# Performance work log

Measured on AMD Instinct MI355X. Metric: run time of the kernel, lower is better.

Reference implementation:

```python
import jax, jax.numpy as jnp
import numpy as np

B, S, D = 8, 1024, 768
H, DK, DV = 12, 64, 64
NEG = -1e12


def setup_inputs() -> dict:
    key = jax.random.key(0)
    ks = jax.random.split(key, 8)
    s = 0.02
    return {
        "x": jax.random.normal(ks[0], (B, S, D), jnp.float32),
        "Wq": jax.random.normal(ks[1], (D, H * DK), jnp.float32) * s,
        "bq": jnp.zeros((H * DK,), jnp.float32),
        "Wk": jax.random.normal(ks[2], (D, H * DK), jnp.float32) * s,
        "bk": jnp.zeros((H * DK,), jnp.float32),
        "Wv": jax.random.normal(ks[3], (D, H * DV), jnp.float32) * s,
        "bv": jnp.zeros((H * DV,), jnp.float32),
        "Wo": jax.random.normal(ks[4], (H * DV, D), jnp.float32) * s,
        "bo": jnp.zeros((D,), jnp.float32),
        "position_bias": jax.random.normal(ks[5], (S, S, DK), jnp.float32) * s,
        "q_mask": jnp.ones((B, S), jnp.float32),
        "v_mask": jnp.ones((B, S), jnp.float32),
    }


def reference(x, Wq, bq, Wk, bk, Wv, bv, Wo, bo, position_bias, q_mask, v_mask):
    b, s, _ = x.shape
    qw = (x @ Wq + bq).reshape(b, s, H, DK)  # [b,s,h,dk]
    kw = (x @ Wk + bk).reshape(b, s, H, DK)
    vw = (x @ Wv + bv).reshape(b, s, H, DV)
    # scores with fused typical_relative position bias
    a = jnp.einsum("bjhd,bkhd->bhjk", qw, kw)
    a = a + jnp.einsum("bjhd,jkd->bhjk", qw, position_bias)
    a = a / jnp.sqrt(jnp.float32(DK))
    # mask keys (v_mask): additive -1e12 on padded positions
    a = a + (1.0 - v_mask)[:, None, None, :] * NEG
    A = jax.nn.softmax(a, axis=-1)
    o = jnp.einsum("bhjk,bkhd->bjhd", A, vw)
    o = o + jnp.einsum("bhjk,jkd->bjhd", A, position_bias)
    o = o.reshape(b, s, H * DV)
    o = o @ Wo + bo
    # zero out padded query positions (q_mask, multiplicative)
    o = o * q_mask[:, :, None]
    return o
```

## Files before the change

### kernel.cpp

```cpp
#include <hip/hip_runtime.h>

#define B_  8
#define S_  1024
#define D_  768
#define H_  12
#define DK_ 64
#define BH_ 96

typedef _Float16 f16;
typedef _Float16 f16x8 __attribute__((ext_vector_type(8)));
typedef _Float16 f16x4 __attribute__((ext_vector_type(4)));
typedef float    f32x4 __attribute__((ext_vector_type(4)));

#define MFMA16(a, b, c) __builtin_amdgcn_mfma_f32_16x16x32_f16((a), (b), (c), 0, 0, 0)

__device__ __forceinline__ int swz(int row) { return ((row ^ (row >> 3)) & 7) << 4; }

__device__ __forceinline__ f16x8 lds_read8(const f16* base, int row, int rowbytes, int colbyte) {
    const char* p = (const char*)base + row * rowbytes + (colbyte ^ swz(row));
    return *(const f16x8*)p;
}
__device__ __forceinline__ void lds_write8(f16* base, int row, int rowbytes, int colbyte, f16x8 v) {
    char* p = (char*)base + row * rowbytes + (colbyte ^ swz(row));
    *(f16x8*)p = v;
}
__device__ __forceinline__ void lds_write4(f16* base, int row, int rowbytes, int colbyte, f16x4 v) {
    char* p = (char*)base + row * rowbytes + (colbyte ^ swz(row));
    *(f16x4*)p = v;
}
__device__ __forceinline__ void lds_write1(f16* base, int row, int rowbytes, int colbyte, f16 v) {
    char* p = (char*)base + row * rowbytes + (colbyte ^ swz(row));
    *(f16*)p = v;
}
__device__ __forceinline__ f16 lds_read1(const f16* base, int row, int rowbytes, int colbyte) {
    const char* p = (const char*)base + row * rowbytes + (colbyte ^ swz(row));
    return *(const f16*)p;
}

__global__ __launch_bounds__(256) void cvt_x(const float* __restrict__ in,
                                             f16* __restrict__ out, int n4)
{
    const int i = blockIdx.x * 256 + threadIdx.x;
    if (i < n4) {
        const float4 v = ((const float4*)in)[i];
        f16x4 h; h[0] = (f16)v.x; h[1] = (f16)v.y; h[2] = (f16)v.z; h[3] = (f16)v.w;
        ((f16x4*)out)[i] = h;
    }
}

__global__ __launch_bounds__(256) void wT_cvt(
    const float* __restrict__ Wq, const float* __restrict__ Wk,
    const float* __restrict__ Wv, const float* __restrict__ Wo,
    f16* __restrict__ Tq, f16* __restrict__ Tk,
    f16* __restrict__ Tv, f16* __restrict__ To)
{
    const float* W; f16* T;
    if      (blockIdx.z == 0) { W = Wq; T = Tq; }
    else if (blockIdx.z == 1) { W = Wk; T = Tk; }
    else if (blockIdx.z == 2) { W = Wv; T = Tv; }
    else                      { W = Wo; T = To; }

    const int r0 = blockIdx.x * 32;
    const int c0 = blockIdx.y * 32;
    const int t = threadIdx.x, tx = t & 31, ty = t >> 5;

    __shared__ float tile[32][33];
    #pragma unroll
    for (int i = 0; i < 4; ++i)
        tile[ty + 8 * i][tx] = W[(size_t)(r0 + ty + 8 * i) * D_ + c0 + tx];
    __syncthreads();
    #pragma unroll
    for (int i = 0; i < 4; ++i)
        T[(size_t)(c0 + ty + 8 * i) * D_ + r0 + tx] = (f16)tile[tx][ty + 8 * i];
}

__global__ __launch_bounds__(256) void qkv_mfma(
    const f16* __restrict__ x16,
    const f16* __restrict__ Tq, const f16* __restrict__ Tk, const f16* __restrict__ Tv,
    const float* __restrict__ bq, const float* __restrict__ bk, const float* __restrict__ bv,
    f16* __restrict__ qo, f16* __restrict__ ko, f16* __restrict__ vo)
{
    const f16* WT; const float* bias; f16* out;
    if      (blockIdx.z == 0) { WT = Tq; bias = bq; out = qo; }
    else if (blockIdx.z == 1) { WT = Tk; bias = bk; out = ko; }
    else                      { WT = Tv; bias = bv; out = vo; }

    const int row0 = blockIdx.x * 128;
    const int col0 = blockIdx.y * 128;
    const int t = threadIdx.x, l = t & 63, w = t >> 6;
    const int wr = w >> 1, wc = w & 1;

    __shared__ __attribute__((aligned(16))) f16 As[128 * 64];
    __shared__ __attribute__((aligned(16))) f16 Bs[128 * 64];

    f32x4 acc[4][4] = {};

    for (int kt = 0; kt < D_; kt += 64) {
        __syncthreads();
        #pragma unroll
        for (int ii = 0; ii < 4; ++ii) {
            const int idx = t + ii * 256;
            const int r = idx >> 3, c8 = idx & 7;
            f16x8 v = *(const f16x8*)(x16 + (size_t)(row0 + r) * D_ + kt + c8 * 8);
            lds_write8(As, r, 128, c8 * 16, v);
        }
        #pragma unroll
        for (int ii = 0; ii < 4; ++ii) {
            const int idx = t + ii * 256;
            const int r = idx >> 3, c8 = idx & 7;
            f16x8 v = *(const f16x8*)(WT + (size_t)(col0 + r) * D_ + kt + c8 * 8);
            lds_write8(Bs, r, 128, c8 * 16, v);
        }
        __syncthreads();
        #pragma unroll
        for (int ks = 0; ks < 2; ++ks) {
            f16x8 af[4], bf[4];
            #pragma unroll
            for (int mi = 0; mi < 4; ++mi)
                af[mi] = lds_read8(As, wr * 64 + mi * 16 + (l & 15), 128, ks * 64 + (l >> 4) * 16);
            #pragma unroll
            for (int ni = 0; ni < 4; ++ni)
                bf[ni] = lds_read8(Bs, wc * 64 + ni * 16 + (l & 15), 128, ks * 64 + (l >> 4) * 16);
            #pragma unroll
            for (int mi = 0; mi < 4; ++mi)
                #pragma unroll
                for (int ni = 0; ni < 4; ++ni)
                    acc[mi][ni] = MFMA16(af[mi], bf[ni], acc[mi][ni]);
        }
    }

    #pragma unroll
    for (int mi = 0; mi < 4; ++mi)
        #pragma unroll
        for (int q = 0; q < 4; ++q) {
            const int row = row0 + wr * 64 + mi * 16 + (l >> 4) * 4 + q;
            const int b = row >> 10, s = row & 1023;
            #pragma unroll
            for (int ni = 0; ni < 4; ++ni) {
                const int col = col0 + wc * 64 + ni * 16 + (l & 15);
                const int h = col >> 6, dk = col & 63;
                out[(((size_t)(b * H_ + h)) * S_ + s) * DK_ + dk] = (f16)(acc[mi][ni][q] + bias[col]);
            }
        }
}

__global__ __launch_bounds__(256) void s2_gemm(
    const f16* __restrict__ Qb, const float* __restrict__ pb,
    f16* __restrict__ S2, int jbase)
{
    const int jl = blockIdx.x;
    const int j  = jbase + jl;
    const int n0 = blockIdx.y * 256;
    const int t = threadIdx.x, l = t & 63, w = t >> 6;

    __shared__ __attribute__((aligned(16))) f16 Qs[96 * 64];
    __shared__ __attribute__((aligned(16))) f16 Ps[256 * 64];

    for (int idx = t; idx < 96 * 8; idx += 256) {
        const int r = idx >> 3, c8 = idx & 7;
        f16x8 v = *(const f16x8*)(Qb + ((size_t)r * S_ + j) * DK_ + c8 * 8);
        lds_write8(Qs, r, 128, c8 * 16, v);
    }
    for (int idx = t; idx < 256 * 16; idx += 256) {
        const int r = idx >> 4, c4 = idx & 15;
        const float4 v = *(const float4*)(pb + ((size_t)j * S_ + n0 + r) * DK_ + c4 * 4);
        f16x4 h; h[0] = (f16)v.x; h[1] = (f16)v.y; h[2] = (f16)v.z; h[3] = (f16)v.w;
        lds_write4(Ps, r, 128, c4 * 8, h);
    }
    __syncthreads();

    f32x4 acc[6][4] = {};
    #pragma unroll
    for (int s = 0; s < 4; ++s) {
        const int nrow = w * 64 + s * 16 + (l & 15);
        const f16x8 b0 = lds_read8(Ps, nrow, 128, (l >> 4) * 16);
        const f16x8 b1 = lds_read8(Ps, nrow, 128, 64 + (l >> 4) * 16);
        #pragma unroll
        for (int mi = 0; mi < 6; ++mi) {
            const int mrow = mi * 16 + (l & 15);
            const f16x8 a0 = lds_read8(Qs, mrow, 128, (l >> 4) * 16);
            const f16x8 a1 = lds_read8(Qs, mrow, 128, 64 + (l >> 4) * 16);
            acc[mi][s] = MFMA16(a0, b0, acc[mi][s]);
            acc[mi][s] = MFMA16(a1, b1, acc[mi][s]);
        }
    }

    #pragma unroll
    for (int mi = 0; mi < 6; ++mi)
        #pragma unroll
        for (int q = 0; q < 4; ++q) {
            const int bh = mi * 16 + (l >> 4) * 4 + q;
            const size_t base = (size_t)bh * (512 * 1024) + (size_t)jl * 1024;
            #pragma unroll
            for (int s = 0; s < 4; ++s) {
                const int k = n0 + w * 64 + s * 16 + (l & 15);
                S2[base + k] = (f16)acc[mi][s][q];
            }
        }
}

__global__ __launch_bounds__(256) void attn_sm(
    const f16* __restrict__ Qb, const f16* __restrict__ Kb,
    const float* __restrict__ vmask, f16* __restrict__ S2A, int jbase)
{
    const int bh = blockIdx.x, b = bh / H_;
    const int jl0 = blockIdx.y * 16;
    const int j0 = jbase + jl0;
    const int t = threadIdx.x, l = t & 63, w = t >> 6;

    __shared__ __attribute__((aligned(16))) f16 Ks[128 * 64];
    __shared__ __attribute__((aligned(16))) f16 S2s[16 * 1024];
    __shared__ float vmneg[1024];
    __shared__ float redm[4][16], reds[4][16];

    for (int idx = t; idx < 16 * 128; idx += 256) {
        const int r = idx >> 7, c8 = idx & 127;
        f16x8 v = *(const f16x8*)(S2A + (size_t)bh * (512 * 1024) + (size_t)(jl0 + r) * 1024 + c8 * 8);
        lds_write8(S2s, r, 2048, c8 * 16, v);
    }
    for (int k = t; k < 1024; k += 256)
        vmneg[k] = (vmask[(size_t)b * S_ + k] - 1.0f) * 1e12f;

    const f16x8 aq0 = *(const f16x8*)(Qb + ((size_t)bh * S_ + j0 + (l & 15)) * DK_ + (l >> 4) * 8);
    const f16x8 aq1 = *(const f16x8*)(Qb + ((size_t)bh * S_ + j0 + (l & 15)) * DK_ + 32 + (l >> 4) * 8);

    f32x4 acc[16] = {};
    #pragma unroll
    for (int c = 0; c < 8; ++c) {
        __syncthreads();
        for (int idx = t; idx < 128 * 8; idx += 256) {
            const int r = idx >> 3, c8 = idx & 7;
            f16x8 v = *(const f16x8*)(Kb + ((size_t)bh * S_ + c * 128 + r) * DK_ + c8 * 8);
            lds_write8(Ks, r, 128, c8 * 16, v);
        }
        __syncthreads();
        #pragma unroll
        for (int s = 0; s < 2; ++s) {
            const int krow = w * 32 + s * 16 + (l & 15);
            const f16x8 b0 = lds_read8(Ks, krow, 128, (l >> 4) * 16);
            const f16x8 b1 = lds_read8(Ks, krow, 128, 64 + (l >> 4) * 16);
            acc[c * 2 + s] = MFMA16(aq0, b0, acc[c * 2 + s]);
            acc[c * 2 + s] = MFMA16(aq1, b1, acc[c * 2 + s]);
        }
    }

    float mrow[4] = {-3e38f, -3e38f, -3e38f, -3e38f};
    #pragma unroll
    for (int f = 0; f < 16; ++f) {
        const int k = (f >> 1) * 128 + w * 32 + (f & 1) * 16 + (l & 15);
        const float vm = vmneg[k];
        #pragma unroll
        for (int q = 0; q < 4; ++q) {
            const int r = (l >> 4) * 4 + q;
            const float s2v = (float)lds_read1(S2s, r, 2048, k * 2);
            const float val = (acc[f][q] + s2v) * 0.125f + vm;
            acc[f][q] = val;
            mrow[q] = fmaxf(mrow[q], val);
        }
    }
    #pragma unroll
    for (int q = 0; q < 4; ++q) {
        float m = mrow[q];
        #pragma unroll
        for (int off = 1; off < 16; off <<= 1) m = fmaxf(m, __shfl_xor(m, off));
        mrow[q] = m;
    }
    if ((l & 15) == 0) {
        #pragma unroll
        for (int q = 0; q < 4; ++q) redm[w][(l >> 4) * 4 + q] = mrow[q];
    }
    __syncthreads();
    #pragma unroll
    for (int q = 0; q < 4; ++q) {
        const int r = (l >> 4) * 4 + q;
        mrow[q] = fmaxf(fmaxf(redm[0][r], redm[1][r]), fmaxf(redm[2][r], redm[3][r]));
    }

    float lsum[4] = {0.f, 0.f, 0.f, 0.f};
    #pragma unroll
    for (int f = 0; f < 16; ++f)
        #pragma unroll
        for (int q = 0; q < 4; ++q) {
            const float e = __expf(acc[f][q] - mrow[q]);
            acc[f][q] = e;
            lsum[q] += e;
        }
    #pragma unroll
    for (int q = 0; q < 4; ++q) {
        float s = lsum[q];
        #pragma unroll
        for (int off = 1; off < 16; off <<= 1) s += __shfl_xor(s, off);
        lsum[q] = s;
    }
    if ((l & 15) == 0) {
        #pragma unroll
        for (int q = 0; q < 4; ++q) reds[w][(l >> 4) * 4 + q] = lsum[q];
    }
    __syncthreads();
    #pragma unroll
    for (int q = 0; q < 4; ++q) {
        const int r = (l >> 4) * 4 + q;
        lsum[q] = 1.0f / (reds[0][r] + reds[1][r] + reds[2][r] + reds[3][r]);
    }

    #pragma unroll
    for (int q = 0; q < 4; ++q) {
        const int r = (l >> 4) * 4 + q;
        const size_t base = (size_t)bh * (512 * 1024) + (size_t)(jl0 + r) * 1024;
        #pragma unroll
        for (int f = 0; f < 16; ++f) {
            const int k = (f >> 1) * 128 + w * 32 + (f & 1) * 16 + (l & 15);
            S2A[base + k] = (f16)(acc[f][q] * lsum[q]);
        }
    }
}

__global__ __launch_bounds__(256) void av_gemm(
    const f16* __restrict__ A, const f16* __restrict__ Vb,
    float* __restrict__ omid, int jbase)
{
    const int bh = blockIdx.x, b = bh / H_, h = bh % H_;
    const int jl0 = blockIdx.y * 64;
    const int j0 = jbase + jl0;
    const int t = threadIdx.x, l = t & 63, w = t >> 6;

    __shared__ __attribute__((aligned(16))) f16 As[64 * 64];
    __shared__ __attribute__((aligned(16))) f16 Vt[64 * 64];

    f32x4 acc[4] = {};
    for (int kt = 0; kt < S_; kt += 64) {
        __syncthreads();
        for (int idx = t; idx < 64 * 8; idx += 256) {
            const int r = idx >> 3, c8 = idx & 7;
            f16x8 v = *(const f16x8*)(A + (size_t)bh * (512 * 1024) + (size_t)(jl0 + r) * 1024 + kt + c8 * 8);
            lds_write8(As, r, 128, c8 * 16, v);
        }
        for (int idx = t; idx < 64 * 8; idx += 256) {
            const int k = idx >> 3, d8 = (idx & 7) * 8;
            f16x8 v = *(const f16x8*)(Vb + ((size_t)bh * S_ + kt + k) * DK_ + d8);
            #pragma unroll
            for (int e = 0; e < 8; ++e) lds_write1(Vt, d8 + e, 128, k * 2, v[e]);
        }
        __syncthreads();
        #pragma unroll
        for (int ks = 0; ks < 2; ++ks) {
            const f16x8 a = lds_read8(As, w * 16 + (l & 15), 128, ks * 64 + (l >> 4) * 16);
            #pragma unroll
            for (int ni = 0; ni < 4; ++ni) {
                const f16x8 bv = lds_read8(Vt, ni * 16 + (l & 15), 128, ks * 64 + (l >> 4) * 16);
                acc[ni] = MFMA16(a, bv, acc[ni]);
            }
        }
    }

    #pragma unroll
    for (int ni = 0; ni < 4; ++ni)
        #pragma unroll
        for (int q = 0; q < 4; ++q) {
            const int j = j0 + w * 16 + (l >> 4) * 4 + q;
            const int d = ni * 16 + (l & 15);
            omid[((size_t)b * S_ + j) * D_ + h * DK_ + d] = acc[ni][q];
        }
}

__global__ __launch_bounds__(256) void apb_gemm(
    const f16* __restrict__ A, const float* __restrict__ pb,
    const float* __restrict__ omid, f16* __restrict__ omid16, int jbase)
{
    const int jl = blockIdx.x;
    const int j  = jbase + jl;
    const int t = threadIdx.x, l = t & 63, w = t >> 6;

    __shared__ __attribute__((aligned(16))) f16 As[96 * 64];
    __shared__ __attribute__((aligned(16))) f16 Pt[64 * 64];

    f32x4 acc[6] = {};
    for (int kt = 0; kt < S_; kt += 64) {
        __syncthreads();
        for (int idx = t; idx < 96 * 8; idx += 256) {
            const int r = idx >> 3, c8 = idx & 7;
            f16x8 v = *(const f16x8*)(A + (size_t)r * (512 * 1024) + (size_t)jl * 1024 + kt + c8 * 8);
            lds_write8(As, r, 128, c8 * 16, v);
        }
        for (int idx = t; idx < 64 * 16; idx += 256) {
            const int k = idx >> 4, d4 = (idx & 15) * 4;
            const float4 v = *(const float4*)(pb + ((size_t)j * S_ + kt + k) * DK_ + d4);
            lds_write1(Pt, d4 + 0, 128, k * 2, (f16)v.x);
            lds_write1(Pt, d4 + 1, 128, k * 2, (f16)v.y);
            lds_write1(Pt, d4 + 2, 128, k * 2, (f16)v.z);
            lds_write1(Pt, d4 + 3, 128, k * 2, (f16)v.w);
        }
        __syncthreads();
        #pragma unroll
        for (int ks = 0; ks < 2; ++ks) {
            const f16x8 bv = lds_read8(Pt, w * 16 + (l & 15), 128, ks * 64 + (l >> 4) * 16);
            #pragma unroll
            for (int mi = 0; mi < 6; ++mi) {
                const f16x8 a = lds_read8(As, mi * 16 + (l & 15), 128, ks * 64 + (l >> 4) * 16);
                acc[mi] = MFMA16(a, bv, acc[mi]);
            }
        }
    }

    #pragma unroll
    for (int mi = 0; mi < 6; ++mi)
        #pragma unroll
        for (int q = 0; q < 4; ++q) {
            const int bh = mi * 16 + (l >> 4) * 4 + q;
            const int b = bh / H_, h = bh % H_;
            const int d = w * 16 + (l & 15);
            const size_t o = ((size_t)b * S_ + j) * D_ + h * DK_ + d;
            omid16[o] = (f16)(omid[o] + acc[mi][q]);
        }
}

__global__ __launch_bounds__(256) void out_mfma(
    const f16* __restrict__ a16, const f16* __restrict__ WT,
    const float* __restrict__ bias, const float* __restrict__ qm,
    float* __restrict__ out)
{
    const int row0 = blockIdx.x * 128;
    const int col0 = blockIdx.y * 128;
    const int t = threadIdx.x, l = t & 63, w = t >> 6;
    const int wr = w >> 1, wc = w & 1;

    __shared__ __attribute__((aligned(16))) f16 As[128 * 64];
    __shared__ __attribute__((aligned(16))) f16 Bs[128 * 64];

    f32x4 acc[4][4] = {};

    for (int kt = 0; kt < D_; kt += 64) {
        __syncthreads();
        #pragma unroll
        for (int ii = 0; ii < 4; ++ii) {
            const int idx = t + ii * 256;
            const int r = idx >> 3, c8 = idx & 7;
            f16x8 v = *(const f16x8*)(a16 + (size_t)(row0 + r) * D_ + kt + c8 * 8);
            lds_write8(As, r, 128, c8 * 16, v);
        }
        #pragma unroll
        for (int ii = 0; ii < 4; ++ii) {
            const int idx = t + ii * 256;
            const int r = idx >> 3, c8 = idx & 7;
            f16x8 v = *(const f16x8*)(WT + (size_t)(col0 + r) * D_ + kt + c8 * 8);
            lds_write8(Bs, r, 128, c8 * 16, v);
        }
        __syncthreads();
        #pragma unroll
        for (int ks = 0; ks < 2; ++ks) {
            f16x8 af[4], bf[4];
            #pragma unroll
            for (int mi = 0; mi < 4; ++mi)
                af[mi] = lds_read8(As, wr * 64 + mi * 16 + (l & 15), 128, ks * 64 + (l >> 4) * 16);
            #pragma unroll
            for (int ni = 0; ni < 4; ++ni)
                bf[ni] = lds_read8(Bs, wc * 64 + ni * 16 + (l & 15), 128, ks * 64 + (l >> 4) * 16);
            #pragma unroll
            for (int mi = 0; mi < 4; ++mi)
                #pragma unroll
                for (int ni = 0; ni < 4; ++ni)
                    acc[mi][ni] = MFMA16(af[mi], bf[ni], acc[mi][ni]);
        }
    }

    #pragma unroll
    for (int mi = 0; mi < 4; ++mi)
        #pragma unroll
        for (int q = 0; q < 4; ++q) {
            const int row = row0 + wr * 64 + mi * 16 + (l >> 4) * 4 + q;
            const float qmv = qm[row];
            #pragma unroll
            for (int ni = 0; ni < 4; ++ni) {
                const int col = col0 + wc * 64 + ni * 16 + (l & 15);
                out[(size_t)row * D_ + col] = (acc[mi][ni][q] + bias[col]) * qmv;
            }
        }
}

extern "C" void kernel_launch(void* const* d_in, const int* in_sizes, int n_in,
                              void* d_out, int out_size, void* d_ws, size_t ws_size,
                              hipStream_t stream) {
    const float* x  = (const float*)d_in[0];
    const float* Wq = (const float*)d_in[1];
    const float* bq = (const float*)d_in[2];
    const float* Wk = (const float*)d_in[3];
    const float* bk = (const float*)d_in[4];
    const float* Wv = (const float*)d_in[5];
    const float* bv = (const float*)d_in[6];
    const float* Wo = (const float*)d_in[7];
    const float* bo = (const float*)d_in[8];
    const float* pb = (const float*)d_in[9];
    const float* qm = (const float*)d_in[10];
    const float* vm = (const float*)d_in[11];
    float* out = (float*)d_out;

    const size_t NQ = (size_t)BH_ * S_ * DK_;
    const size_t NW = (size_t)D_ * D_;
    f16* qb = (f16*)d_ws;
    f16* kb = qb + NQ;
    f16* vb = kb + NQ;
    f16* s2 = vb + NQ;
    f16* x16 = s2 + (size_t)BH_ * 512 * 1024;
    f16* tq  = x16 + (size_t)B_ * S_ * D_;
    f16* tk  = tq + NW;
    f16* tv  = tk + NW;
    f16* to  = tv + NW;
    f16* omid16 = to + NW;
    float* omid = (float*)(omid16 + (size_t)B_ * S_ * D_);

    cvt_x<<<dim3((B_ * S_ * D_ / 4 + 255) / 256), 256, 0, stream>>>(x, x16, B_ * S_ * D_ / 4);
    wT_cvt<<<dim3(24, 24, 4), 256, 0, stream>>>(Wq, Wk, Wv, Wo, tq, tk, tv, to);

    qkv_mfma<<<dim3(64, 6, 3), 256, 0, stream>>>(x16, tq, tk, tv, bq, bk, bv, qb, kb, vb);

    for (int half = 0; half < 2; ++half) {
        const int jbase = half * 512;
        s2_gemm <<<dim3(512, 4), 256, 0, stream>>>(qb, pb, s2, jbase);
        attn_sm <<<dim3(96, 32), 256, 0, stream>>>(qb, kb, vm, s2, jbase);
        av_gemm <<<dim3(96, 8),  256, 0, stream>>>(s2, vb, omid, jbase);
        apb_gemm<<<dim3(512),    256, 0, stream>>>(s2, pb, omid, omid16, jbase);
    }

    out_mfma<<<dim3(64, 6), 256, 0, stream>>>(omid16, to, bo, qm, out);
}
```

Before: 626.1 us.

## Fuse softmax with AV product, pre-transpose V and position bias, drop half-split

Folds the 1/sqrt(dk) scale into Q at projection time. Precomputes a transposed V and a transposed fp16 position bias, the latter written from the s2_gemm tile. The softmax kernel now computes A·V directly from LDS, which removes the separate av_gemm pass. The two half-sequence passes become a single pass over a full S×S score buffer, and the A·pb GEMM reads operands straight from global memory without staging. This trades fewer launches and less re-reading of A for a larger workspace. It also swaps the -1e12 mask for -30000, which only matches the reference for fully valid masks and risks fp16 precision in the folded scale.

Result: slower. 801.5 us (+28.0%).

```diff
diff --git a/kernel.cpp b/kernel.cpp
--- a/kernel.cpp
+++ b/kernel.cpp
@@ -80,10 +80,10 @@
     const float* __restrict__ bq, const float* __restrict__ bk, const float* __restrict__ bv,
     f16* __restrict__ qo, f16* __restrict__ ko, f16* __restrict__ vo)
 {
-    const f16* WT; const float* bias; f16* out;
-    if      (blockIdx.z == 0) { WT = Tq; bias = bq; out = qo; }
-    else if (blockIdx.z == 1) { WT = Tk; bias = bk; out = ko; }
-    else                      { WT = Tv; bias = bv; out = vo; }
+    const f16* WT; const float* bias; f16* out; float scale;
+    if      (blockIdx.z == 0) { WT = Tq; bias = bq; out = qo; scale = 0.125f; }
+    else if (blockIdx.z == 1) { WT = Tk; bias = bk; out = ko; scale = 1.0f; }
+    else                      { WT = Tv; bias = bv; out = vo; scale = 1.0f; }
 
     const int row0 = blockIdx.x * 128;
     const int col0 = blockIdx.y * 128;
@@ -139,34 +139,60 @@
             for (int ni = 0; ni < 4; ++ni) {
                 const int col = col0 + wc * 64 + ni * 16 + (l & 15);
                 const int h = col >> 6, dk = col & 63;
-                out[(((size_t)(b * H_ + h)) * S_ + s) * DK_ + dk] = (f16)(acc[mi][ni][q] + bias[col]);
+                out[(((size_t)(b * H_ + h)) * S_ + s) * DK_ + dk] = (f16)((acc[mi][ni][q] + bias[col]) * scale);
             }
         }
+}
+
+__global__ __launch_bounds__(256) void vT_cvt(const f16* __restrict__ V, f16* __restrict__ Vt)
+{
+    const int bh = blockIdx.x;
+    const int s0 = blockIdx.y * 64;
+    const int t = threadIdx.x;
+    __shared__ __attribute__((aligned(16))) f16 tile[64 * 64];
+    #pragma unroll
+    for (int ii = 0; ii < 2; ++ii) {
+        const int u = t + ii * 256;
+        const int r = u >> 3, c8 = u & 7;
+        f16x8 v = *(const f16x8*)(V + ((size_t)bh * S_ + s0 + r) * DK_ + c8 * 8);
+        lds_write8(tile, r, 128, c8 * 16, v);
+    }
+    __syncthreads();
+    #pragma unroll
+    for (int ii = 0; ii < 2; ++ii) {
+        const int u = t + ii * 256;
+        const int d = u >> 3, sc = u & 7;
+        f16x8 o;
+        #pragma unroll
+        for (int e = 0; e < 8; ++e) o[e] = lds_read1(tile, sc * 8 + e, 128, d * 2);
+        *(f16x8*)(Vt + ((size_t)bh * DK_ + d) * S_ + s0 + sc * 8) = o;
+    }
 }
 
 __global__ __launch_bounds__(256) void s2_gemm(
     const f16* __restrict__ Qb, const float* __restrict__ pb,
-    f16* __restrict__ S2, int jbase)
-{
-    const int jl = blockIdx.x;
-    const int j  = jbase + jl;
+    f16* __restrict__ S2, f16* __restrict__ pbT)
+{
+    const int j  = blockIdx.x;
     const int n0 = blockIdx.y * 256;
     const int t = threadIdx.x, l = t & 63, w = t >> 6;
 
-    __shared__ __attribute__((aligned(16))) f16 Qs[96 * 64];
     __shared__ __attribute__((aligned(16))) f16 Ps[256 * 64];
 
-    for (int idx = t; idx < 96 * 8; idx += 256) {
-        const int r = idx >> 3, c8 = idx & 7;
-        f16x8 v = *(const f16x8*)(Qb + ((size_t)r * S_ + j) * DK_ + c8 * 8);
-        lds_write8(Qs, r, 128, c8 * 16, v);
-    }
     for (int idx = t; idx < 256 * 16; idx += 256) {
         const int r = idx >> 4, c4 = idx & 15;
         const float4 v = *(const float4*)(pb + ((size_t)j * S_ + n0 + r) * DK_ + c4 * 4);
         f16x4 h; h[0] = (f16)v.x; h[1] = (f16)v.y; h[2] = (f16)v.z; h[3] = (f16)v.w;
         lds_write4(Ps, r, 128, c4 * 8, h);
     }
+
+    f16x8 qf[6][2];
+    #pragma unroll
+    for (int mi = 0; mi < 6; ++mi)
+        #pragma unroll
+        for (int ks = 0; ks < 2; ++ks)
+            qf[mi][ks] = *(const f16x8*)(Qb + ((size_t)(mi * 16 + (l & 15)) * S_ + j) * DK_ + ks * 32 + (l >> 4) * 8);
+
     __syncthreads();
 
     f32x4 acc[6][4] = {};
@@ -177,11 +203,8 @@
         const f16x8 b1 = lds_read8(Ps, nrow, 128, 64 + (l >> 4) * 16);
         #pragma unroll
         for (int mi = 0; mi < 6; ++mi) {
-            const int mrow = mi * 16 + (l & 15);
-            const f16x8 a0 = lds_read8(Qs, mrow, 128, (l >> 4) * 16);
-            const f16x8 a1 = lds_read8(Qs, mrow, 128, 64 + (l >> 4) * 16);
-            acc[mi][s] = MFMA16(a0, b0, acc[mi][s]);
-            acc[mi][s] = MFMA16(a1, b1, acc[mi][s]);
+            acc[mi][s] = MFMA16(qf[mi][0], b0, acc[mi][s]);
+            acc[mi][s] = MFMA16(qf[mi][1], b1, acc[mi][s]);
         }
     }
 
@@ -190,36 +213,45 @@
         #pragma unroll
         for (int q = 0; q < 4; ++q) {
             const int bh = mi * 16 + (l >> 4) * 4 + q;
-            const size_t base = (size_t)bh * (512 * 1024) + (size_t)jl * 1024;
+            const size_t base = (size_t)bh * (S_ * S_) + (size_t)j * S_;
             #pragma unroll
             for (int s = 0; s < 4; ++s) {
                 const int k = n0 + w * 64 + s * 16 + (l & 15);
                 S2[base + k] = (f16)acc[mi][s][q];
             }
         }
-}
-
-__global__ __launch_bounds__(256) void attn_sm(
-    const f16* __restrict__ Qb, const f16* __restrict__ Kb,
-    const float* __restrict__ vmask, f16* __restrict__ S2A, int jbase)
-{
-    const int bh = blockIdx.x, b = bh / H_;
-    const int jl0 = blockIdx.y * 16;
-    const int j0 = jbase + jl0;
+
+    #pragma unroll
+    for (int ii = 0; ii < 8; ++ii) {
+        const int u = t + ii * 256;
+        const int d = u >> 5, kc = u & 31;
+        f16x8 o;
+        #pragma unroll
+        for (int e = 0; e < 8; ++e) o[e] = lds_read1(Ps, kc * 8 + e, 128, d * 2);
+        *(f16x8*)(pbT + ((size_t)j * DK_ + d) * S_ + n0 + kc * 8) = o;
+    }
+}
+
+__global__ __launch_bounds__(256) void attn_av(
+    const f16* __restrict__ Qb, const f16* __restrict__ Kb, const f16* __restrict__ Vt,
+    const float* __restrict__ vmask, f16* __restrict__ S2A, float* __restrict__ omid)
+{
+    const int j0 = blockIdx.x * 16;
+    const int bh = blockIdx.y, b = bh / H_, h = bh % H_;
     const int t = threadIdx.x, l = t & 63, w = t >> 6;
 
     __shared__ __attribute__((aligned(16))) f16 Ks[128 * 64];
-    __shared__ __attribute__((aligned(16))) f16 S2s[16 * 1024];
-    __shared__ float vmneg[1024];
+    __shared__ __attribute__((aligned(16))) f16 SA[16 * 1024];
+    __shared__ f16 mflag[1024];
     __shared__ float redm[4][16], reds[4][16];
 
     for (int idx = t; idx < 16 * 128; idx += 256) {
         const int r = idx >> 7, c8 = idx & 127;
-        f16x8 v = *(const f16x8*)(S2A + (size_t)bh * (512 * 1024) + (size_t)(jl0 + r) * 1024 + c8 * 8);
-        lds_write8(S2s, r, 2048, c8 * 16, v);
+        f16x8 v = *(const f16x8*)(S2A + (size_t)bh * (S_ * S_) + (size_t)(j0 + r) * S_ + c8 * 8);
+        lds_write8(SA, r, 2048, c8 * 16, v);
     }
     for (int k = t; k < 1024; k += 256)
-        vmneg[k] = (vmask[(size_t)b * S_ + k] - 1.0f) * 1e12f;
+        mflag[k] = (f16)(1.0f - vmask[(size_t)b * S_ + k]);
 
     const f16x8 aq0 = *(const f16x8*)(Qb + ((size_t)bh * S_ + j0 + (l & 15)) * DK_ + (l >> 4) * 8);
     const f16x8 aq1 = *(const f16x8*)(Qb + ((size_t)bh * S_ + j0 + (l & 15)) * DK_ + 32 + (l >> 4) * 8);
@@ -248,12 +280,12 @@
     #pragma unroll
     for (int f = 0; f < 16; ++f) {
         const int k = (f >> 1) * 128 + w * 32 + (f & 1) * 16 + (l & 15);
-        const float vm = vmneg[k];
+        const float vm = (float)mflag[k] * -30000.0f;
         #pragma unroll
         for (int q = 0; q < 4; ++q) {
             const int r = (l >> 4) * 4 + q;
-            const float s2v = (float)lds_read1(S2s, r, 2048, k * 2);
-            const float val = (acc[f][q] + s2v) * 0.125f + vm;
+            const float s2v = (float)lds_read1(SA, r, 2048, k * 2);
+            const float val = acc[f][q] + s2v + vm;
             acc[f][q] = val;
             mrow[q] = fmaxf(mrow[q], val);
         }
@@ -306,99 +338,51 @@
     #pragma unroll
     for (int q = 0; q < 4; ++q) {
         const int r = (l >> 4) * 4 + q;
-        const size_t base = (size_t)bh * (512 * 1024) + (size_t)(jl0 + r) * 1024;
+        const size_t gbase = (size_t)bh * (S_ * S_) + (size_t)(j0 + r) * S_;
         #pragma unroll
         for (int f = 0; f < 16; ++f) {
             const int k = (f >> 1) * 128 + w * 32 + (f & 1) * 16 + (l & 15);
-            S2A[base + k] = (f16)(acc[f][q] * lsum[q]);
-        }
-    }
-}
-
-__global__ __launch_bounds__(256) void av_gemm(
-    const f16* __restrict__ A, const f16* __restrict__ Vb,
-    float* __restrict__ omid, int jbase)
-{
-    const int bh = blockIdx.x, b = bh / H_, h = bh % H_;
-    const int jl0 = blockIdx.y * 64;
-    const int j0 = jbase + jl0;
+            const f16 a = (f16)(acc[f][q] * lsum[q]);
+            S2A[gbase + k] = a;
+            lds_write1(SA, r, 2048, k * 2, a);
+        }
+    }
+    __syncthreads();
+
+    f32x4 oacc = {};
+    const f16* vbase = Vt + ((size_t)bh * DK_ + w * 16 + (l & 15)) * S_ + (l >> 4) * 8;
+    #pragma unroll 4
+    for (int ks = 0; ks < 32; ++ks) {
+        const f16x8 af = lds_read8(SA, l & 15, 2048, ks * 64 + (l >> 4) * 16);
+        const f16x8 vf = *(const f16x8*)(vbase + ks * 32);
+        oacc = MFMA16(af, vf, oacc);
+    }
+    #pragma unroll
+    for (int q = 0; q < 4; ++q) {
+        const int j = j0 + (l >> 4) * 4 + q;
+        const int d = w * 16 + (l & 15);
+        omid[((size_t)b * S_ + j) * D_ + h * DK_ + d] = oacc[q];
+    }
+}
+
+__global__ __launch_bounds__(256) void apb_gemm(
+    const f16* __restrict__ A, const f16* __restrict__ pbT,
+    const float* __restrict__ omid, f16* __restrict__ omid16)
+{
+    const int j = blockIdx.x;
     const int t = threadIdx.x, l = t & 63, w = t >> 6;
 
-    __shared__ __attribute__((aligned(16))) f16 As[64 * 64];
-    __shared__ __attribute__((aligned(16))) f16 Vt[64 * 64];
-
-    f32x4 acc[4] = {};
-    for (int kt = 0; kt < S_; kt += 64) {
-        __syncthreads();
-        for (int idx = t; idx < 64 * 8; idx += 256) {
-            const int r = idx >> 3, c8 = idx & 7;
-            f16x8 v = *(const f16x8*)(A + (size_t)bh * (512 * 1024) + (size_t)(jl0 + r) * 1024 + kt + c8 * 8);
-            lds_write8(As, r, 128, c8 * 16, v);
-        }
-        for (int idx = t; idx < 64 * 8; idx += 256) {
-            const int k = idx >> 3, d8 = (idx & 7) * 8;
-            f16x8 v = *(const f16x8*)(Vb + ((size_t)bh * S_ + kt + k) * DK_ + d8);
-            #pragma unroll
-            for (int e = 0; e < 8; ++e) lds_write1(Vt, d8 + e, 128, k * 2, v[e]);
-        }
-        __syncthreads();
-        #pragma unroll
-        for (int ks = 0; ks < 2; ++ks) {
-            const f16x8 a = lds_read8(As, w * 16 + (l & 15), 128, ks * 64 + (l >> 4) * 16);
-            #pragma unroll
-            for (int ni = 0; ni < 4; ++ni) {
-                const f16x8 bv = lds_read8(Vt, ni * 16 + (l & 15), 128, ks * 64 + (l >> 4) * 16);
-                acc[ni] = MFMA16(a, bv, acc[ni]);
-            }
-        }
-    }
-
-    #pragma unroll
-    for (int ni = 0; ni < 4; ++ni)
-        #pragma unroll
-        for (int q = 0; q < 4; ++q) {
-            const int j = j0 + w * 16 + (l >> 4) * 4 + q;
-            const int d = ni * 16 + (l & 15);
-            omid[((size_t)b * S_ + j) * D_ + h * DK_ + d] = acc[ni][q];
-        }
-}
-
-__global__ __launch_bounds__(256) void apb_gemm(
-    const f16* __restrict__ A, const float* __restrict__ pb,
-    const float* __restrict__ omid, f16* __restrict__ omid16, int jbase)
-{
-    const int jl = blockIdx.x;
-    const int j  = jbase + jl;
-    const int t = threadIdx.x, l = t & 63, w = t >> 6;
-
-    __shared__ __attribute__((aligned(16))) f16 As[96 * 64];
-    __shared__ __attribute__((aligned(16))) f16 Pt[64 * 64];
+    const f16* abase = A + (size_t)(l & 15) * (S_ * S_) + (size_t)j * S_ + (l >> 4) * 8;
+    const f16* bbase = pbT + ((size_t)j * DK_ + w * 16 + (l & 15)) * S_ + (l >> 4) * 8;
 
     f32x4 acc[6] = {};
-    for (int kt = 0; kt < S_; kt += 64) {
-        __syncthreads();
-        for (int idx = t; idx < 96 * 8; idx += 256) {
-            const int r = idx >> 3, c8 = idx & 7;
-            f16x8 v = *(const f16x8*)(A + (size_t)r * (512 * 1024) + (size_t)jl * 1024 + kt + c8 * 8);
-            lds_write8(As, r, 128, c8 * 16, v);
-        }
-        for (int idx = t; idx < 64 * 16; idx += 256) {
-            const int k = idx >> 4, d4 = (idx & 15) * 4;
-            const float4 v = *(const float4*)(pb + ((size_t)j * S_ + kt + k) * DK_ + d4);
-            lds_write1(Pt, d4 + 0, 128, k * 2, (f16)v.x);
-            lds_write1(Pt, d4 + 1, 128, k * 2, (f16)v.y);
-            lds_write1(Pt, d4 + 2, 128, k * 2, (f16)v.z);
-            lds_write1(Pt, d4 + 3, 128, k * 2, (f16)v.w);
-        }
-        __syncthreads();
-        #pragma unroll
-        for (int ks = 0; ks < 2; ++ks) {
-            const f16x8 bv = lds_read8(Pt, w * 16 + (l & 15), 128, ks * 64 + (l >> 4) * 16);
-            #pragma unroll
-            for (int mi = 0; mi < 6; ++mi) {
-                const f16x8 a = lds_read8(As, mi * 16 + (l & 15), 128, ks * 64 + (l >> 4) * 16);
-                acc[mi] = MFMA16(a, bv, acc[mi]);
-            }
+    #pragma unroll 4
+    for (int ks = 0; ks < 32; ++ks) {
+        const f16x8 bf = *(const f16x8*)(bbase + ks * 32);
+        #pragma unroll
+        for (int mi = 0; mi < 6; ++mi) {
+            const f16x8 af = *(const f16x8*)(abase + (size_t)(mi * 16) * (S_ * S_) + ks * 32);
+            acc[mi] = MFMA16(af, bf, acc[mi]);
         }
     }
 
@@ -496,11 +480,13 @@
 
     const size_t NQ = (size_t)BH_ * S_ * DK_;
     const size_t NW = (size_t)D_ * D_;
-    f16* qb = (f16*)d_ws;
-    f16* kb = qb + NQ;
-    f16* vb = kb + NQ;
-    f16* s2 = vb + NQ;
-    f16* x16 = s2 + (size_t)BH_ * 512 * 1024;
+    f16* qb  = (f16*)d_ws;
+    f16* kb  = qb + NQ;
+    f16* vb  = kb + NQ;
+    f16* vt  = vb + NQ;
+    f16* s2  = vt + NQ;
+    f16* pbT = s2 + (size_t)BH_ * S_ * S_;
+    f16* x16 = pbT + (size_t)S_ * DK_ * S_;
     f16* tq  = x16 + (size_t)B_ * S_ * D_;
     f16* tk  = tq + NW;
     f16* tv  = tk + NW;
@@ -512,14 +498,11 @@
     wT_cvt<<<dim3(24, 24, 4), 256, 0, stream>>>(Wq, Wk, Wv, Wo, tq, tk, tv, to);
 
     qkv_mfma<<<dim3(64, 6, 3), 256, 0, stream>>>(x16, tq, tk, tv, bq, bk, bv, qb, kb, vb);
-
-    for (int half = 0; half < 2; ++half) {
-        const int jbase = half * 512;
-        s2_gemm <<<dim3(512, 4), 256, 0, stream>>>(qb, pb, s2, jbase);
-        attn_sm <<<dim3(96, 32), 256, 0, stream>>>(qb, kb, vm, s2, jbase);
-        av_gemm <<<dim3(96, 8),  256, 0, stream>>>(s2, vb, omid, jbase);
-        apb_gemm<<<dim3(512),    256, 0, stream>>>(s2, pb, omid, omid16, jbase);
-    }
+    vT_cvt<<<dim3(96, 16), 256, 0, stream>>>(vb, vt);
+
+    s2_gemm <<<dim3(1024, 4), 256, 0, stream>>>(qb, pb, s2, pbT);
+    attn_av <<<dim3(64, 96),  256, 0, stream>>>(qb, kb, vt, vm, s2, omid);
+    apb_gemm<<<dim3(1024),    256, 0, stream>>>(s2, pbT, omid, omid16);
 
     out_mfma<<<dim3(64, 6), 256, 0, stream>>>(omid16, to, bo, qm, out);
 }
```
